# Optimization experiments

Hardware: AMD Instinct MI355X
Metric: run time of the kernel (lower is better)

## Reference

```python
import jax, jax.numpy as jnp
import numpy as np

# pywt db4 decomposition filters (dec_lo / dec_hi), exactly as pywt.Wavelet('db4')
DEC_LO = np.array([-0.010597401784997278, 0.032883011666982945, 0.030841381835986965,
                   -0.18703481171888114, -0.02798376941698385, 0.6308807679295904,
                   0.7148465705525415, 0.23037781330885523], dtype=np.float32)
DEC_HI = np.array([-0.23037781330885523, 0.7148465705525415, -0.6308807679295904,
                   -0.02798376941698385, 0.18703481171888114, 0.030841381835986965,
                   -0.032883011666982945, -0.010597401784997278], dtype=np.float32)

PATCH_LEN, STRIDE, PAD = 8, 4, 4


def _dwt(x, lo_rev, hi_rev):
    """Single-level pywt dwt with mode='symmetric' along last axis.
    pywt: out[i] = sum_j h[j] * x_ext[2i+1-j]  ->  correlate reversed filter
    with symmetric-extended signal starting at offset 1."""
    F = lo_rev.shape[0]  # 8
    n = x.shape[-1]
    out_len = (n + F - 1) // 2
    ext = jnp.pad(x, [(0, 0)] * (x.ndim - 1) + [(F - 1, F - 1)], mode='symmetric')
    # window index matrix: (out_len, F), windows start at 1, 3, 5, ...
    idx = 1 + 2 * np.arange(out_len)[:, None] + np.arange(F)[None, :]
    win = ext[..., idx]                      # (..., out_len, F)
    return win @ lo_rev, win @ hi_rev        # (cA, cD)


def setup_inputs() -> dict:
    key = jax.random.key(0)
    k1, k2 = jax.random.split(key)
    B, C, T, V = 32, 3, 4096, 25
    x = jax.random.normal(k1, (B, C, T, V), dtype=jnp.float32)
    # nn.Linear(in=C*28, out=128, bias=False) weight, (out, in) layout
    W = jax.random.normal(k2, (128, C * 28), dtype=jnp.float32) * (1.0 / np.sqrt(C * 28))
    return {"x": x, "W": W}


def reference(x, W):
    B, C, T, V = x.shape
    # ReplicationPad2d((0,0,0,PAD)) pads end of time axis (dim -2) by edge replication
    xp = jnp.pad(x, ((0, 0), (0, 0), (0, PAD), (0, 0)), mode='edge')
    P = (T + PAD - PATCH_LEN) // STRIDE + 1
    widx = STRIDE * np.arange(P)[:, None] + np.arange(PATCH_LEN)  # (P, L)
    xw = xp[:, :, widx, :]                   # (B, C, P, L, V)
    xw = xw.transpose(0, 4, 2, 1, 3)         # (B, V, P, C, L) == torch permute(0,3,2,1,4)

    lo_rev = jnp.asarray(DEC_LO[::-1].copy())
    hi_rev = jnp.asarray(DEC_HI[::-1].copy())
    cA, cD = _dwt(xw, lo_rev, hi_rev)        # each (B, V, P, C, 7)
    aa, ad = _dwt(cA, lo_rev, hi_rev)        # level-2 nodes of approx
    da, dd = _dwt(cD, lo_rev, hi_rev)        # level-2 nodes of detail
    y = jnp.concatenate([aa, ad, dd, da], axis=-1)  # (B, V, P, C, 28)
    y = y.reshape(B, V * P, C * 28)
    return y @ W.T                           # (B, V*P, 128)
```

## Files before the change

### kernel.cpp

```cpp
#include <hip/hip_runtime.h>
#include <hip/hip_bf16.h>

struct M28x8 { float m[28][8]; };

constexpr double DLO[8] = {-0.010597401784997278, 0.032883011666982945,
                            0.030841381835986965, -0.18703481171888114,
                           -0.02798376941698385,   0.6308807679295904,
                            0.7148465705525415,    0.23037781330885523};
constexpr double DHI[8] = {-0.23037781330885523,   0.7148465705525415,
                           -0.6308807679295904,   -0.02798376941698385,
                            0.18703481171888114,   0.030841381835986965,
                           -0.032883011666982945, -0.010597401784997278};

constexpr void dwt_c(const double* x, int n, double* lo, double* hi) {
    int out_len = (n + 7) / 2;
    for (int i = 0; i < out_len; ++i) {
        double a = 0.0, d = 0.0;
        for (int j = 0; j < 8; ++j) {
            int q = 2 * i + j - 6;
            if (q < 0) q = -q - 1;
            if (q >= n) q = 2 * n - 1 - q;
            a += DLO[7 - j] * x[q];
            d += DHI[7 - j] * x[q];
        }
        lo[i] = a; hi[i] = d;
    }
}

constexpr M28x8 build_M() {
    M28x8 R{};
    for (int j = 0; j < 8; ++j) {
        double x[8] = {0,0,0,0,0,0,0,0};
        x[j] = 1.0;
        double cA[7] = {}, cD[7] = {};
        dwt_c(x, 8, cA, cD);
        double aa[7] = {}, ad[7] = {}, da[7] = {}, dd[7] = {};
        dwt_c(cA, 7, aa, ad);
        dwt_c(cD, 7, da, dd);
        for (int i = 0; i < 7; ++i) {
            R.m[i][j]      = (float)aa[i];
            R.m[7 + i][j]  = (float)ad[i];
            R.m[14 + i][j] = (float)dd[i];
            R.m[21 + i][j] = (float)da[i];
        }
    }
    return R;
}

__constant__ M28x8 g_M = build_M();

__global__ void wfold_kernel(const float* __restrict__ W, float* __restrict__ Wf) {
    int t = blockIdx.x * blockDim.x + threadIdx.x;
    if (t >= 128 * 24) return;
    int o = t / 24;
    int cj = t - o * 24;
    int c = cj >> 3;
    int j = cj & 7;
    const float* wr = W + o * 84 + c * 28;
    float acc = 0.f;
#pragma unroll
    for (int k = 0; k < 28; ++k) acc += wr[k] * g_M.m[k][j];
    Wf[t] = acc;
}

#define PT   16
#define TT   (4 * PT + 4)
#define SLAB (3 * 25 * TT)

__global__ __launch_bounds__(256, 2) void wave_kernel(const float* __restrict__ x,
                                                      const float* __restrict__ Wf,
                                                      float* __restrict__ out) {
    __shared__ float s_x[SLAB];
    const int tile = blockIdx.x;
    const int b    = blockIdx.y;
    const int t0   = tile * (4 * PT);
    const int tid  = threadIdx.x;

    for (int lin = tid; lin < SLAB; lin += 256) {
        int v  = lin % 25;
        int r  = lin / 25;
        int tt = r % TT;
        int c  = r / TT;
        int t  = t0 + tt;
        if (t > 4095) t = 4095;
        s_x[(c * 25 + v) * TT + tt] = x[((b * 3 + c) * 4096 + t) * 25 + v];
    }

    const int og  = tid & 31;
    const int grp = tid >> 5;
    const int o   = og << 2;

    float wr[4][24];
#pragma unroll
    for (int m = 0; m < 4; ++m) {
        const float4* wp = (const float4*)(Wf + (o + m) * 24);
#pragma unroll
        for (int q = 0; q < 6; ++q) {
            float4 f = wp[q];
            wr[m][4 * q + 0] = f.x; wr[m][4 * q + 1] = f.y;
            wr[m][4 * q + 2] = f.z; wr[m][4 * q + 3] = f.w;
        }
    }

    __syncthreads();

    const long out_blk = (long)(b * 25600 + tile * PT) * 128 + o;
    for (int idx = grp; idx < 25 * PT; idx += 8) {
        const int v  = idx >> 4;
        const int pl = idx & 15;
        float acc[4] = {0.f, 0.f, 0.f, 0.f};
#pragma unroll
        for (int c = 0; c < 3; ++c) {
            const float4* row = (const float4*)(s_x + (c * 25 + v) * TT + 4 * pl);
            float4 xa = row[0];
            float4 xb = row[1];
#pragma unroll
            for (int m = 0; m < 4; ++m) {
                acc[m] += wr[m][c*8+0]*xa.x + wr[m][c*8+1]*xa.y
                        + wr[m][c*8+2]*xa.z + wr[m][c*8+3]*xa.w
                        + wr[m][c*8+4]*xb.x + wr[m][c*8+5]*xb.y
                        + wr[m][c*8+6]*xb.z + wr[m][c*8+7]*xb.w;
            }
        }
        float4 st = {acc[0], acc[1], acc[2], acc[3]};
        *(float4*)(out + out_blk + (long)(v * 1024 + pl) * 128) = st;
    }
}

extern "C" void kernel_launch(void* const* d_in, const int* in_sizes, int n_in,
                              void* d_out, int out_size, void* d_ws, size_t ws_size,
                              hipStream_t stream) {
    const float* x = (const float*)d_in[0];
    const float* W = (const float*)d_in[1];
    float* out = (float*)d_out;
    float* Wf  = (float*)d_ws;

    hipLaunchKernelGGL(wfold_kernel, dim3(12), dim3(256), 0, stream, W, Wf);
    hipLaunchKernelGGL(wave_kernel, dim3(64, 32), dim3(256), 0, stream, x, Wf, out);
}
```

Measured before the change: 471.4 us.

## Give each lane one patch, read wave-uniform folded weights, loop outputs

Each lane now owns one patch and holds its 24 inputs in registers. It loops over all 128 outputs, reading the folded weights as wave-uniform values instead of keeping per-thread weight registers. The time tile grows to 64 patches with 320-thread blocks, one wave per channel group, and the grid shrinks to 16x32 blocks. This is meant to cut redundant shared-memory reads and per-thread weight registers. In exchange, lanes store float4s strided by 512 bytes instead of as one contiguous row, and far fewer waves are resident because of the larger LDS slab and the smaller grid.

```diff
diff --git a/kernel.cpp b/kernel.cpp
--- a/kernel.cpp
+++ b/kernel.cpp
@@ -63,11 +63,11 @@
     Wf[t] = acc;
 }
 
-#define PT   16
-#define TT   (4 * PT + 4)
-#define SLAB (3 * 25 * TT)
+#define PT    64
+#define TT    (4 * PT + 4)
+#define SLAB  (3 * 25 * TT)
 
-__global__ __launch_bounds__(256, 2) void wave_kernel(const float* __restrict__ x,
+__global__ __launch_bounds__(320, 2) void wave_kernel(const float* __restrict__ x,
                                                       const float* __restrict__ Wf,
                                                       float* __restrict__ out) {
     __shared__ float s_x[SLAB];
@@ -76,7 +76,7 @@
     const int t0   = tile * (4 * PT);
     const int tid  = threadIdx.x;
 
-    for (int lin = tid; lin < SLAB; lin += 256) {
+    for (int lin = tid; lin < SLAB; lin += 320) {
         int v  = lin % 25;
         int r  = lin / 25;
         int tt = r % TT;
@@ -86,44 +86,39 @@
         s_x[(c * 25 + v) * TT + tt] = x[((b * 3 + c) * 4096 + t) * 25 + v];
     }
 
-    const int og  = tid & 31;
-    const int grp = tid >> 5;
-    const int o   = og << 2;
-
-    float wr[4][24];
-#pragma unroll
-    for (int m = 0; m < 4; ++m) {
-        const float4* wp = (const float4*)(Wf + (o + m) * 24);
-#pragma unroll
-        for (int q = 0; q < 6; ++q) {
-            float4 f = wp[q];
-            wr[m][4 * q + 0] = f.x; wr[m][4 * q + 1] = f.y;
-            wr[m][4 * q + 2] = f.z; wr[m][4 * q + 3] = f.w;
-        }
-    }
+    const int lane = tid & 63;
+    const int wv   = tid >> 6;
 
     __syncthreads();
 
-    const long out_blk = (long)(b * 25600 + tile * PT) * 128 + o;
-    for (int idx = grp; idx < 25 * PT; idx += 8) {
-        const int v  = idx >> 4;
-        const int pl = idx & 15;
-        float acc[4] = {0.f, 0.f, 0.f, 0.f};
+    for (int g = 0; g < 5; ++g) {
+        const int v = wv + 5 * g;
+
+        float xw[24];
 #pragma unroll
         for (int c = 0; c < 3; ++c) {
-            const float4* row = (const float4*)(s_x + (c * 25 + v) * TT + 4 * pl);
-            float4 xa = row[0];
-            float4 xb = row[1];
+            const float4* wp = (const float4*)(s_x + (c * 25 + v) * TT + 4 * lane);
+            float4 xa = wp[0];
+            float4 xb = wp[1];
+            xw[c*8+0] = xa.x; xw[c*8+1] = xa.y; xw[c*8+2] = xa.z; xw[c*8+3] = xa.w;
+            xw[c*8+4] = xb.x; xw[c*8+5] = xb.y; xw[c*8+6] = xb.z; xw[c*8+7] = xb.w;
+        }
+
+        float* op = out + ((long)(b * 25600 + v * 1024 + tile * PT + lane)) * 128;
+
+        for (int och = 0; och < 32; ++och) {
+            const float* wrow = Wf + och * 96;
+            float a0 = 0.f, a1 = 0.f, a2 = 0.f, a3 = 0.f;
 #pragma unroll
-            for (int m = 0; m < 4; ++m) {
-                acc[m] += wr[m][c*8+0]*xa.x + wr[m][c*8+1]*xa.y
-                        + wr[m][c*8+2]*xa.z + wr[m][c*8+3]*xa.w
-                        + wr[m][c*8+4]*xb.x + wr[m][c*8+5]*xb.y
-                        + wr[m][c*8+6]*xb.z + wr[m][c*8+7]*xb.w;
+            for (int i = 0; i < 24; ++i) {
+                a0 += wrow[i]      * xw[i];
+                a1 += wrow[24 + i] * xw[i];
+                a2 += wrow[48 + i] * xw[i];
+                a3 += wrow[72 + i] * xw[i];
             }
+            float4 st = {a0, a1, a2, a3};
+            *(float4*)(op + och * 4) = st;
         }
-        float4 st = {acc[0], acc[1], acc[2], acc[3]};
-        *(float4*)(out + out_blk + (long)(v * 1024 + pl) * 128) = st;
     }
 }
 
@@ -136,5 +131,5 @@
     float* Wf  = (float*)d_ws;
 
     hipLaunchKernelGGL(wfold_kernel, dim3(12), dim3(256), 0, stream, W, Wf);
-    hipLaunchKernelGGL(wave_kernel, dim3(64, 32), dim3(256), 0, stream, x, Wf, out);
+    hipLaunchKernelGGL(wave_kernel, dim3(16, 32), dim3(320), 0, stream, x, Wf, out);
 }
```

New measurement: 844.2 us. 79.1% more time.
